# Optimization experiments

Measured on AMD Instinct MI355X. Metric: run time of the kernel, lower is better.

## Reference

```python
import jax, jax.numpy as jnp
import numpy as np

B, C, H, W = 4, 512, 64, 64
MID = C // 8  # 64


def setup_inputs() -> dict:
    key = jax.random.key(0)
    ks = jax.random.split(key, 8)
    s = 0.02
    return {
        "x": jax.random.normal(ks[0], (B, C, H, W), dtype=jnp.float32),
        "Wq": jax.random.normal(ks[1], (MID, C), dtype=jnp.float32) * s,
        "bq": jax.random.normal(ks[2], (MID,), dtype=jnp.float32) * s,
        "Wk": jax.random.normal(ks[3], (MID, C), dtype=jnp.float32) * s,
        "bk": jax.random.normal(ks[4], (MID,), dtype=jnp.float32) * s,
        "Wv": jax.random.normal(ks[5], (C, C), dtype=jnp.float32) * s,
        "bv": jax.random.normal(ks[6], (C,), dtype=jnp.float32) * s,
        "gamma": jax.random.uniform(ks[7], (1,), dtype=jnp.float32),
    }


def reference(x, Wq, bq, Wk, bk, Wv, bv, gamma):
    b, c, h, w = x.shape
    n = h * w
    xf = x.reshape(b, c, n)  # [B, C, N]
    # 1x1 convs are per-position linear maps
    q = jnp.einsum('mc,bcn->bnm', Wq, xf) + bq            # [B, N, mid]
    k = jnp.einsum('mc,bcn->bmn', Wk, xf) + bk[:, None]   # [B, mid, N]
    sim = jax.nn.softmax(jnp.einsum('bnm,bmj->bnj', q, k), axis=-1)  # [B, N, N]
    v = jnp.einsum('dc,bcn->bdn', Wv, xf) + bv[:, None]   # [B, C, N]
    # feat[:, d, i] = sum_j v[:, d, j] * sim[:, i, j]
    feat = jnp.einsum('bdj,bij->bdi', v, sim)             # [B, C, N]
    out = gamma[0] * feat + xf
    return out.reshape(b, c, h, w)
```

## Files before the change

kernel.cpp:

```cpp
#include <hip/hip_runtime.h>

#define BATCH 4
#define CCH   512
#define NN    4096
#define MIDD  64

typedef unsigned short u16;
typedef unsigned int   u32;
typedef short s8v  __attribute__((ext_vector_type(8)));
typedef float f16v __attribute__((ext_vector_type(16)));

__device__ __forceinline__ u16 f2bf(float f) {
  u32 u = __float_as_uint(f);
  u += 0x7fffu + ((u >> 16) & 1u);
  return (u16)(u >> 16);
}

__device__ __forceinline__ void g2lds16(const u16* g, u16* l) {
  __builtin_amdgcn_global_load_lds(
      (const __attribute__((address_space(1))) u32*)(const void*)g,
      (__attribute__((address_space(3))) u32*)(void*)l, 16, 0, 0);
}

#define S_WAITCNT(vm, lgkm) \
  __builtin_amdgcn_s_waitcnt(((vm) & 15) | (((vm) >> 4) << 14) | (0x7 << 4) | ((lgkm) << 8))

__global__ __launch_bounds__(256) void transpose_cast(
    const float* __restrict__ x, u16* __restrict__ xbT)
{
  const int b  = blockIdx.z;
  const int c0 = blockIdx.y * 64;
  const int n0 = blockIdx.x * 64;
  const int t  = threadIdx.x;
  __shared__ float ts[64 * 65];

  #pragma unroll
  for (int k = 0; k < 4; k++) {
    int idx = t + 256 * k;
    int cc = idx >> 4, n4 = idx & 15;
    float4 v = *(const float4*)&x[((size_t)(b * CCH + c0 + cc)) * NN + n0 + n4 * 4];
    float* p = &ts[cc * 65 + n4 * 4];
    p[0] = v.x; p[1] = v.y; p[2] = v.z; p[3] = v.w;
  }
  __syncthreads();

  const int n = t >> 2, cb = (t & 3) * 16;
  u16 tmp[16];
  #pragma unroll
  for (int j = 0; j < 16; j++) tmp[j] = f2bf(ts[(cb + j) * 65 + n]);
  u16* dst = &xbT[((size_t)b * NN + n0 + n) * CCH + c0 + cb];
  *(uint4*)&dst[0] = *(uint4*)&tmp[0];
  *(uint4*)&dst[8] = *(uint4*)&tmp[8];
}

__global__ __launch_bounds__(256, 2) void proj_gemm(
    const u16* __restrict__ xbT,
    const float* __restrict__ Wq, const float* __restrict__ bq,
    const float* __restrict__ Wk, const float* __restrict__ bk,
    const float* __restrict__ Wv, const float* __restrict__ bv,
    u16* __restrict__ qT, u16* __restrict__ kT, u16* __restrict__ vT)
{
  const int b  = blockIdx.z;
  const int mt = blockIdx.y;
  const int n0 = blockIdx.x * 256;
  const int t  = threadIdx.x;
  const int ln = t & 31, hi = (t & 63) >> 5, w = t >> 6;
  const int l  = t & 63, l3 = l & 7, lh3 = l >> 3;

  const float* W; const float* bias;
  if (mt < 8)       { W = Wv + (size_t)mt * 64 * CCH; bias = bv + mt * 64; }
  else if (mt == 8) { W = Wq; bias = bq; }
  else              { W = Wk; bias = bk; }

  __shared__ u16 ws[64 * 72];
  __shared__ u16 xs[256 * 64];

  const u16* xsrc = xbT + ((size_t)b * NN + n0 + w * 64 + lh3) * CCH + (l3 ^ lh3) * 8;

  f16v acc[4];
  #pragma unroll
  for (int i = 0; i < 4; i++)
    #pragma unroll
    for (int r = 0; r < 16; r++) acc[i][r] = 0.f;

  for (int c0 = 0; c0 < CCH; c0 += 64) {
    __syncthreads();
    #pragma unroll
    for (int k = 0; k < 4; k++) {
      int idx = t + 256 * k;
      int mm = idx >> 4, c4 = (idx & 15) * 4;
      float4 v = *(const float4*)&W[(size_t)mm * CCH + c0 + c4];
      uint2 p;
      p.x = (u32)f2bf(v.x) | ((u32)f2bf(v.y) << 16);
      p.y = (u32)f2bf(v.z) | ((u32)f2bf(v.w) << 16);
      *(uint2*)&ws[mm * 72 + c4] = p;
    }
    #pragma unroll
    for (int i = 0; i < 8; i++)
      g2lds16(xsrc + (size_t)(8 * i) * CCH + c0, xs + (w * 8 + i) * 512);
    __syncthreads();

    #pragma unroll
    for (int ks = 0; ks < 4; ks++) {
      const int cb = ((2 * ks + hi) ^ l3) << 3;
      s8v a0 = *(const s8v*)&ws[(0  + ln) * 72 + hi * 8 + 16 * ks];
      s8v a1 = *(const s8v*)&ws[(32 + ln) * 72 + hi * 8 + 16 * ks];
      s8v b0 = *(const s8v*)&xs[((w * 64 + 0  + ln) << 6) + cb];
      s8v b1 = *(const s8v*)&xs[((w * 64 + 32 + ln) << 6) + cb];
      acc[0] = __builtin_amdgcn_mfma_f32_32x32x16_bf16(a0, b0, acc[0], 0, 0, 0);
      acc[1] = __builtin_amdgcn_mfma_f32_32x32x16_bf16(a0, b1, acc[1], 0, 0, 0);
      acc[2] = __builtin_amdgcn_mfma_f32_32x32x16_bf16(a1, b0, acc[2], 0, 0, 0);
      acc[3] = __builtin_amdgcn_mfma_f32_32x32x16_bf16(a1, b1, acc[3], 0, 0, 0);
    }
  }

  if (mt < 8) {
    const int m0g = mt * 64;
    #pragma unroll
    for (int mi = 0; mi < 2; mi++)
      #pragma unroll
      for (int ni = 0; ni < 2; ni++) {
        f16v& a = acc[mi * 2 + ni];
        #pragma unroll
        for (int r = 0; r < 16; r++) {
          int row = (r & 3) + 8 * (r >> 2) + 4 * hi;
          int m   = mi * 32 + row;
          float val = a[r] + bias[m];
          vT[((size_t)b * CCH + m0g + m) * NN + n0 + w * 64 + ni * 32 + ln] = f2bf(val);
        }
      }
  } else {
    u16* dst = (mt == 8) ? qT : kT;
    __syncthreads();
    u16* xt = (u16*)xs;
    #pragma unroll
    for (int mi = 0; mi < 2; mi++)
      #pragma unroll
      for (int ni = 0; ni < 2; ni++) {
        f16v& a = acc[mi * 2 + ni];
        #pragma unroll
        for (int r = 0; r < 16; r++) {
          int row = (r & 3) + 8 * (r >> 2) + 4 * hi;
          int m   = mi * 32 + row;
          int nr = w * 64 + ni * 32 + ln;
          xt[(nr << 6) + (((m >> 3) ^ (ln & 7)) << 3) + (m & 7)] = f2bf(a[r] + bias[m]);
        }
      }
    __syncthreads();
    const int r7 = t & 7;
    u16* drow = &dst[((size_t)b * NN + n0 + t) * 64];
    #pragma unroll
    for (int k = 0; k < 8; k++)
      *(uint4*)&drow[k * 8] = *(uint4*)&xt[(t << 6) + ((k ^ r7) << 3)];
  }
}

__global__ __launch_bounds__(256, 2) void attn_kernel(
    const u16* __restrict__ qT,
    const u16* __restrict__ kT,
    const u16* __restrict__ vT,
    const float* __restrict__ x,
    const float* __restrict__ gamma,
    float* __restrict__ out)
{
  __shared__ u16 ksm[2][64 * 64];
  __shared__ u16 plm[2][64 * 64];
  __shared__ u16 vsm[256 * 64];

  const int bx    = blockIdx.x;
  const int slot  = bx & 7;
  const int b     = slot >> 1;
  const int dbase = (slot & 1) * 256;
  const int i0    = (bx >> 3) * 64;
  const int t     = threadIdx.x;
  const int l     = t & 63, ln = l & 31, hi = l >> 5;
  const int w     = t >> 6;
  const int qh    = w >> 1;
  const int jh    = w & 1;
  const int l3    = l & 7, lh3 = l >> 3;
  const int sw8   = (l3 ^ lh3) * 8;

  s8v qfrag[4];
  {
    const u16* qp = qT + ((size_t)b * NN + i0 + qh * 32 + ln) * 64 + hi * 8;
    #pragma unroll
    for (int k = 0; k < 4; k++) qfrag[k] = *(const s8v*)(qp + 16 * k);
  }

  const u16* kbase = kT + (size_t)b * NN * 64;
  const u16* vbase = vT + ((size_t)b * CCH + dbase) * NN;
  const u16* ksrc  = kbase + (size_t)(16 * w + lh3) * 64 + sw8;
  const u16* vsrc  = vbase + (size_t)(64 * w + lh3) * NN + sw8;

  f16v oacc[4];
  #pragma unroll
  for (int i = 0; i < 4; i++)
    #pragma unroll
    for (int r = 0; r < 16; r++) oacc[i][r] = 0.f;
  float lpart[16];
  #pragma unroll
  for (int r = 0; r < 16; r++) lpart[r] = 0.f;

  #pragma unroll
  for (int i = 0; i < 2; i++)
    g2lds16(ksrc + (size_t)(8 * i) * 64, &ksm[0][(w * 2 + i) * 512]);

  for (int it = 0; it < 64; it++) {
    const int j0  = it * 64;
    const int cur = it & 1, nxt = cur ^ 1;

    __builtin_amdgcn_s_barrier();
    #pragma unroll
    for (int i = 0; i < 8; i++)
      g2lds16(vsrc + (size_t)(8 * i) * NN + j0, vsm + (w * 8 + i) * 512);
    const int j1 = ((it + 1) & 63) * 64;
    #pragma unroll
    for (int i = 0; i < 2; i++)
      g2lds16(ksrc + (size_t)(j1 + 8 * i) * 64, &ksm[nxt][(w * 2 + i) * 512]);

    S_WAITCNT(10, 15);
    __builtin_amdgcn_s_barrier();

    f16v sacc;
    #pragma unroll
    for (int r = 0; r < 16; r++) sacc[r] = 0.f;
    #pragma unroll
    for (int ks = 0; ks < 4; ks++) {
      s8v bf = *(const s8v*)&ksm[cur][(jh * 32 + ln) * 64 + (((2 * ks + hi) ^ l3) << 3)];
      sacc = __builtin_amdgcn_mfma_f32_32x32x16_bf16(qfrag[ks], bf, sacc, 0, 0, 0);
    }
    #pragma unroll
    for (int r = 0; r < 16; r++) {
      float p = __expf(sacc[r]);
      lpart[r] += p;
      int row = qh * 32 + (r & 3) + ((r >> 2) << 3) + (hi << 2);
      int r7  = (r & 3) + (hi << 2);
      int jbl = (jh << 2) + (ln >> 3);
      plm[cur][(row << 6) + ((jbl ^ r7) << 3) + (ln & 7)] = f2bf(p);
    }

    S_WAITCNT(2, 0);
    __builtin_amdgcn_s_barrier();

    #pragma unroll
    for (int ks = 0; ks < 4; ks++) {
      const int cb = ((2 * ks + hi) ^ l3) << 3;
      s8v p0 = *(const s8v*)&plm[cur][(ln << 6) + cb];
      s8v p1 = *(const s8v*)&plm[cur][((32 + ln) << 6) + cb];
      s8v v0 = *(const s8v*)&vsm[(((w << 5) + ln) << 6) + cb];
      s8v v1 = *(const s8v*)&vsm[((((w + 4) << 5) + ln) << 6) + cb];
      oacc[0] = __builtin_amdgcn_mfma_f32_32x32x16_bf16(v0, p0, oacc[0], 0, 0, 0);
      oacc[1] = __builtin_amdgcn_mfma_f32_32x32x16_bf16(v0, p1, oacc[1], 0, 0, 0);
      oacc[2] = __builtin_amdgcn_mfma_f32_32x32x16_bf16(v1, p0, oacc[2], 0, 0, 0);
      oacc[3] = __builtin_amdgcn_mfma_f32_32x32x16_bf16(v1, p1, oacc[3], 0, 0, 0);
    }
  }

  S_WAITCNT(0, 0);
  __builtin_amdgcn_s_barrier();

  float* lred = (float*)&ksm[0][0];
  #pragma unroll
  for (int r = 0; r < 16; r++) {
    float v = lpart[r];
    v += __shfl_xor(v, 1);  v += __shfl_xor(v, 2);  v += __shfl_xor(v, 4);
    v += __shfl_xor(v, 8);  v += __shfl_xor(v, 16);
    lpart[r] = v;
  }
  if (ln == 0) {
    #pragma unroll
    for (int r = 0; r < 16; r++) {
      int row = qh * 32 + (r & 3) + ((r >> 2) << 3) + (hi << 2);
      lred[jh * 64 + row] = lpart[r];
    }
  }
  __syncthreads();

  const float g0 = gamma[0];
  #pragma unroll
  for (int qt = 0; qt < 2; qt++) {
    const float linv = 1.0f / (lred[qt * 32 + ln] + lred[64 + qt * 32 + ln]);
    const int n = i0 + qt * 32 + ln;
    #pragma unroll
    for (int ds = 0; ds < 2; ds++) {
      f16v& a = oacc[ds * 2 + qt];
      const int dg = dbase + (w + 4 * ds) * 32;
      #pragma unroll
      for (int r = 0; r < 16; r++) {
        int dl = (r & 3) + 8 * (r >> 2) + 4 * hi;
        size_t idx = ((size_t)b * CCH + dg + dl) * NN + n;
        out[idx] = g0 * a[r] * linv + x[idx];
      }
    }
  }
}

extern "C" void kernel_launch(void* const* d_in, const int* in_sizes, int n_in,
                              void* d_out, int out_size, void* d_ws, size_t ws_size,
                              hipStream_t stream) {
  const float* x     = (const float*)d_in[0];
  const float* Wq    = (const float*)d_in[1];
  const float* bq    = (const float*)d_in[2];
  const float* Wk    = (const float*)d_in[3];
  const float* bk    = (const float*)d_in[4];
  const float* Wv    = (const float*)d_in[5];
  const float* bv    = (const float*)d_in[6];
  const float* gamma = (const float*)d_in[7];
  float* out = (float*)d_out;

  u16* qT  = (u16*)d_ws;
  u16* kT  = qT  + (size_t)BATCH * NN * MIDD;
  u16* vT  = kT  + (size_t)BATCH * NN * MIDD;
  u16* xbT = vT  + (size_t)BATCH * CCH * NN;

  transpose_cast<<<dim3(NN / 64, CCH / 64, BATCH), 256, 0, stream>>>(x, xbT);
  proj_gemm<<<dim3(NN / 256, 10, BATCH), 256, 0, stream>>>(
      xbT, Wq, bq, Wk, bk, Wv, bv, qT, kT, vT);
  attn_kernel<<<dim3(512), 256, 0, stream>>>(qT, kT, vT, x, gamma, out);
}
```

Baseline: 238.4 us.

## Pre-cast weights to bf16 and double-buffer projection GEMM with async LDS loads

Adds a small prep kernel that converts Wq/Wk/Wv to bf16 once per call, so the projection GEMM no longer converts fp32 weights inside its inner loop. The GEMM loop now uses 32-wide K chunks with double-buffered LDS, loading both weights and x through global_load_lds and prefetching the next chunk while the current one computes. This costs an extra kernel launch and a small workspace buffer, and it relies on hand-set waitcnt values and barriers being correct. The epilogue reuses the first x buffer as transpose scratch after a full wait.

```diff
diff --git a/kernel.cpp b/kernel.cpp
--- a/kernel.cpp
+++ b/kernel.cpp
@@ -24,6 +24,25 @@
 
 #define S_WAITCNT(vm, lgkm) \
   __builtin_amdgcn_s_waitcnt(((vm) & 15) | (((vm) >> 4) << 14) | (0x7 << 4) | ((lgkm) << 8))
+
+__global__ __launch_bounds__(256) void prep_w(
+    const float* __restrict__ Wq, const float* __restrict__ Wk,
+    const float* __restrict__ Wv, u16* __restrict__ Wb)
+{
+  int e = (blockIdx.x * 256 + threadIdx.x) * 8;
+  const float* src;
+  if (e < 64 * 512)       src = Wq + e;
+  else if (e < 128 * 512) src = Wk + (e - 64 * 512);
+  else                    src = Wv + (e - 128 * 512);
+  float4 v0 = *(const float4*)src;
+  float4 v1 = *(const float4*)(src + 4);
+  uint4 p;
+  p.x = (u32)f2bf(v0.x) | ((u32)f2bf(v0.y) << 16);
+  p.y = (u32)f2bf(v0.z) | ((u32)f2bf(v0.w) << 16);
+  p.z = (u32)f2bf(v1.x) | ((u32)f2bf(v1.y) << 16);
+  p.w = (u32)f2bf(v1.z) | ((u32)f2bf(v1.w) << 16);
+  *(uint4*)(Wb + e) = p;
+}
 
 __global__ __launch_bounds__(256) void transpose_cast(
     const float* __restrict__ x, u16* __restrict__ xbT)
@@ -54,10 +73,9 @@
 }
 
 __global__ __launch_bounds__(256, 2) void proj_gemm(
-    const u16* __restrict__ xbT,
-    const float* __restrict__ Wq, const float* __restrict__ bq,
-    const float* __restrict__ Wk, const float* __restrict__ bk,
-    const float* __restrict__ Wv, const float* __restrict__ bv,
+    const u16* __restrict__ xbT, const u16* __restrict__ Wb,
+    const float* __restrict__ bq, const float* __restrict__ bk,
+    const float* __restrict__ bv,
     u16* __restrict__ qT, u16* __restrict__ kT, u16* __restrict__ vT)
 {
   const int b  = blockIdx.z;
@@ -65,17 +83,18 @@
   const int n0 = blockIdx.x * 256;
   const int t  = threadIdx.x;
   const int ln = t & 31, hi = (t & 63) >> 5, w = t >> 6;
-  const int l  = t & 63, l3 = l & 7, lh3 = l >> 3;
-
-  const float* W; const float* bias;
-  if (mt < 8)       { W = Wv + (size_t)mt * 64 * CCH; bias = bv + mt * 64; }
-  else if (mt == 8) { W = Wq; bias = bq; }
-  else              { W = Wk; bias = bk; }
-
-  __shared__ u16 ws[64 * 72];
-  __shared__ u16 xs[256 * 64];
-
-  const u16* xsrc = xbT + ((size_t)b * NN + n0 + w * 64 + lh3) * CCH + (l3 ^ lh3) * 8;
+  const int l  = t & 63;
+  const int l2 = l & 3, lr = l >> 2;
+  const int swc = (l2 ^ (lr & 3)) * 8;
+
+  const int mrow0 = (mt < 8) ? (128 + mt * 64) : ((mt == 8) ? 0 : 64);
+  const float* bias = (mt < 8) ? (bv + mt * 64) : ((mt == 8) ? bq : bk);
+
+  __shared__ u16 ws[2][64 * 32];
+  __shared__ u16 xs[2][256 * 32];
+
+  const u16* xsrc = xbT + ((size_t)b * NN + n0 + w * 64 + lr) * CCH + swc;
+  const u16* wsrc = Wb + (size_t)(mrow0 + w * 16 + lr) * 512 + swc;
 
   f16v acc[4];
   #pragma unroll
@@ -83,36 +102,39 @@
     #pragma unroll
     for (int r = 0; r < 16; r++) acc[i][r] = 0.f;
 
-  for (int c0 = 0; c0 < CCH; c0 += 64) {
-    __syncthreads();
-    #pragma unroll
-    for (int k = 0; k < 4; k++) {
-      int idx = t + 256 * k;
-      int mm = idx >> 4, c4 = (idx & 15) * 4;
-      float4 v = *(const float4*)&W[(size_t)mm * CCH + c0 + c4];
-      uint2 p;
-      p.x = (u32)f2bf(v.x) | ((u32)f2bf(v.y) << 16);
-      p.y = (u32)f2bf(v.z) | ((u32)f2bf(v.w) << 16);
-      *(uint2*)&ws[mm * 72 + c4] = p;
-    }
-    #pragma unroll
-    for (int i = 0; i < 8; i++)
-      g2lds16(xsrc + (size_t)(8 * i) * CCH + c0, xs + (w * 8 + i) * 512);
-    __syncthreads();
-
-    #pragma unroll
-    for (int ks = 0; ks < 4; ks++) {
-      const int cb = ((2 * ks + hi) ^ l3) << 3;
-      s8v a0 = *(const s8v*)&ws[(0  + ln) * 72 + hi * 8 + 16 * ks];
-      s8v a1 = *(const s8v*)&ws[(32 + ln) * 72 + hi * 8 + 16 * ks];
-      s8v b0 = *(const s8v*)&xs[((w * 64 + 0  + ln) << 6) + cb];
-      s8v b1 = *(const s8v*)&xs[((w * 64 + 32 + ln) << 6) + cb];
+  #pragma unroll
+  for (int i = 0; i < 4; i++)
+    g2lds16(xsrc + (size_t)(16 * i) * CCH, &xs[0][(w * 64 + i * 16) * 32]);
+  g2lds16(wsrc, &ws[0][w * 16 * 32]);
+
+  for (int it = 0; it < 16; it++) {
+    const int cur = it & 1, nxt = cur ^ 1;
+    __builtin_amdgcn_s_barrier();
+    const int c1 = ((it + 1) & 15) * 32;
+    #pragma unroll
+    for (int i = 0; i < 4; i++)
+      g2lds16(xsrc + (size_t)(16 * i) * CCH + c1, &xs[nxt][(w * 64 + i * 16) * 32]);
+    g2lds16(wsrc + c1, &ws[nxt][w * 16 * 32]);
+
+    S_WAITCNT(5, 15);
+    __builtin_amdgcn_s_barrier();
+
+    #pragma unroll
+    for (int ks = 0; ks < 2; ks++) {
+      const int cb = ((2 * ks + hi) ^ (ln & 3)) << 3;
+      s8v a0 = *(const s8v*)&ws[cur][(ln)           * 32 + cb];
+      s8v a1 = *(const s8v*)&ws[cur][(32 + ln)      * 32 + cb];
+      s8v b0 = *(const s8v*)&xs[cur][(w * 64 + ln)      * 32 + cb];
+      s8v b1 = *(const s8v*)&xs[cur][(w * 64 + 32 + ln) * 32 + cb];
       acc[0] = __builtin_amdgcn_mfma_f32_32x32x16_bf16(a0, b0, acc[0], 0, 0, 0);
       acc[1] = __builtin_amdgcn_mfma_f32_32x32x16_bf16(a0, b1, acc[1], 0, 0, 0);
       acc[2] = __builtin_amdgcn_mfma_f32_32x32x16_bf16(a1, b0, acc[2], 0, 0, 0);
       acc[3] = __builtin_amdgcn_mfma_f32_32x32x16_bf16(a1, b1, acc[3], 0, 0, 0);
     }
   }
+
+  S_WAITCNT(0, 0);
+  __builtin_amdgcn_s_barrier();
 
   if (mt < 8) {
     const int m0g = mt * 64;
@@ -131,8 +153,7 @@
       }
   } else {
     u16* dst = (mt == 8) ? qT : kT;
-    __syncthreads();
-    u16* xt = (u16*)xs;
+    u16* xt  = &xs[0][0];
     #pragma unroll
     for (int mi = 0; mi < 2; mi++)
       #pragma unroll
@@ -142,7 +163,7 @@
         for (int r = 0; r < 16; r++) {
           int row = (r & 3) + 8 * (r >> 2) + 4 * hi;
           int m   = mi * 32 + row;
-          int nr = w * 64 + ni * 32 + ln;
+          int nr  = w * 64 + ni * 32 + ln;
           xt[(nr << 6) + (((m >> 3) ^ (ln & 7)) << 3) + (m & 7)] = f2bf(a[r] + bias[m]);
         }
       }
@@ -312,9 +333,11 @@
   u16* kT  = qT  + (size_t)BATCH * NN * MIDD;
   u16* vT  = kT  + (size_t)BATCH * NN * MIDD;
   u16* xbT = vT  + (size_t)BATCH * CCH * NN;
-
+  u16* Wb  = xbT + (size_t)BATCH * NN * CCH;
+
+  prep_w<<<dim3(160), 256, 0, stream>>>(Wq, Wk, Wv, Wb);
   transpose_cast<<<dim3(NN / 64, CCH / 64, BATCH), 256, 0, stream>>>(x, xbT);
   proj_gemm<<<dim3(NN / 256, 10, BATCH), 256, 0, stream>>>(
-      xbT, Wq, bq, Wk, bk, Wv, bv, qT, kT, vT);
+      xbT, Wb, bq, bk, bv, qT, kT, vT);
   attn_kernel<<<dim3(512), 256, 0, stream>>>(qT, kT, vT, x, gamma, out);
 }
```

Result: no change. 234.1 us (-1.8%).
